# Kernel optimization log

Hardware: AMD Instinct MI355X
Metric: run time of the kernel (lower is better)

Reference implementation:

```python
import jax, jax.numpy as jnp
import numpy as np

D_PAIR = 128
N_HEAD = 4
D_HID = 32
SCALING = 1.0 / np.sqrt(D_HID)


def setup_inputs() -> dict:
    key = jax.random.key(0)
    ks = jax.random.split(key, 12)
    B, L = 1, 256
    s = 0.02
    return {
        "pair": jax.random.normal(ks[0], (B, L, L, D_PAIR), dtype=jnp.float32),
        "gamma": jnp.ones((D_PAIR,), jnp.float32),
        "beta": jnp.zeros((D_PAIR,), jnp.float32),
        "Wq": jax.random.normal(ks[1], (D_PAIR, N_HEAD * D_HID), jnp.float32) * s,
        "Wk": jax.random.normal(ks[2], (D_PAIR, N_HEAD * D_HID), jnp.float32) * s,
        "Wv": jax.random.normal(ks[3], (D_PAIR, N_HEAD * D_HID), jnp.float32) * s,
        "Wb": jax.random.normal(ks[4], (D_PAIR, N_HEAD), jnp.float32) * s,
        "Wg": jax.random.normal(ks[5], (D_PAIR, N_HEAD * D_HID), jnp.float32) * s,
        "bg": jnp.ones((N_HEAD * D_HID,), jnp.float32),
        "Wo": jax.random.normal(ks[6], (N_HEAD * D_HID, D_PAIR), jnp.float32) * s,
        "bo": jnp.zeros((D_PAIR,), jnp.float32),
    }


def _layernorm(x, gamma, beta, eps=1e-5):
    mu = jnp.mean(x, axis=-1, keepdims=True)
    var = jnp.var(x, axis=-1, keepdims=True)
    return (x - mu) * jax.lax.rsqrt(var + eps) * gamma + beta


def reference(pair, gamma, beta, Wq, Wk, Wv, Wb, Wg, bg, Wo, bo):
    B, L = pair.shape[:2]
    x = _layernorm(pair, gamma, beta)                      # (B,L,L,D)
    q = (x @ Wq).reshape(B, L, L, N_HEAD, D_HID) * SCALING  # (B,L,L,h,d)
    k = (x @ Wk).reshape(B, L, L, N_HEAD, D_HID)
    v = (x @ Wv).reshape(B, L, L, N_HEAD, D_HID)
    bias = x @ Wb                                           # (B,L,L,h)
    gate = jax.nn.sigmoid(x @ Wg + bg)                      # (B,L,L,h*d)
    # start_node=True: attend over ending index k of row i
    attn = jnp.einsum('bijhd,bikhd->bijkh', q, k)           # (B,L,L,L,h)
    attn = attn + bias[:, None]                             # bias[b,j,k,h] broadcast over i
    attn = jax.nn.softmax(attn, axis=-2)                    # over k
    out = jnp.einsum('bijkh,bikhd->bijhd', attn, v).reshape(B, L, L, N_HEAD * D_HID)
    out = gate * out
    return out @ Wo + bo
```

## Files before the change

kernel.cpp:

```cpp
#include <hip/hip_runtime.h>
#include <math.h>

#define L 256
#define DP 128
#define NH 4
#define DH 32
#define NROW 65536

typedef unsigned short ushort_t;
typedef __attribute__((ext_vector_type(8))) short short8;
typedef __attribute__((ext_vector_type(4))) float f32x4;
typedef __attribute__((ext_vector_type(4))) unsigned int u32x4;

constexpr float SCALING = 0.17677669529663687f;

static __device__ __forceinline__ unsigned short f2bf(float f) {
    unsigned u = __builtin_bit_cast(unsigned, f);
    u = u + 0x7fffu + ((u >> 16) & 1u);
    return (unsigned short)(u >> 16);
}
static __device__ __forceinline__ float bf2f(unsigned short h) {
    unsigned u = ((unsigned)h) << 16;
    return __builtin_bit_cast(float, u);
}
static __device__ __forceinline__ unsigned packbf(float lo, float hi) {
    return ((unsigned)f2bf(hi) << 16) | (unsigned)f2bf(lo);
}

__global__ __launch_bounds__(256) void prep_kernel(
    const float* __restrict__ Wq, const float* __restrict__ Wk, const float* __restrict__ Wv,
    const float* __restrict__ Wb, const float* __restrict__ Wg, const float* __restrict__ Wo,
    ushort_t* __restrict__ WtAll, ushort_t* __restrict__ WohT, ushort_t* __restrict__ WolT)
{
    int rowi = blockIdx.x * 16 + (threadIdx.x >> 4);
    int d0 = (threadIdx.x & 15) * 8;
    #pragma unroll
    for (int dd = 0; dd < 8; ++dd) {
        int d = d0 + dd;
        if (rowi < 512) {
            int n = rowi & 127;
            float val;
            if (rowi < 128)      val = Wq[d * 128 + n] * SCALING;
            else if (rowi < 256) val = Wk[d * 128 + n];
            else if (rowi < 384) val = Wv[d * 128 + n];
            else                 val = Wg[d * 128 + n];
            WtAll[rowi * 128 + d] = f2bf(val);
        } else if (rowi < 516) {
            WtAll[rowi * 128 + d] = f2bf(Wb[d * 4 + (rowi - 512)]);
        } else if (rowi < 528) {
            WtAll[rowi * 128 + d] = 0;
        } else if (rowi < 656) {
            int n = rowi - 528;
            WohT[n * 128 + d] = f2bf(Wo[d * 128 + n]);
        } else {
            int n = rowi - 656;
            float wv = Wo[d * 128 + n];
            unsigned short hb = f2bf(wv);
            WolT[n * 128 + d] = f2bf(wv - bf2f(hb));
        }
    }
}

__global__ __launch_bounds__(256) void ln_proj_mfma(
    const float* __restrict__ pair, const float* __restrict__ gamma, const float* __restrict__ beta,
    const ushort_t* __restrict__ WtAll, const float* __restrict__ bgv,
    ushort_t* __restrict__ qo, ushort_t* __restrict__ ko, ushort_t* __restrict__ vo,
    ushort_t* __restrict__ gateo, float* __restrict__ biasT)
{
    __shared__ __align__(16) unsigned char xs[32 * 256];

    const int t = threadIdx.x;
    const int w = t >> 6, lane = t & 63;
    const int c = lane & 15, g = lane >> 4;
    const int base = blockIdx.x * 32;

    {
        const float* pr = pair + ((size_t)base + w * 8) * DP;
        float e0[8], e1[8];
        #pragma unroll
        for (int r = 0; r < 8; ++r) {
            e0[r] = pr[r * DP + lane];
            e1[r] = pr[r * DP + 64 + lane];
        }
        const float g0 = gamma[lane], g1 = gamma[lane + 64];
        const float b0 = beta[lane],  b1 = beta[lane + 64];
        #pragma unroll
        for (int r = 0; r < 8; ++r) {
            float s = e0[r] + e1[r], ss = e0[r] * e0[r] + e1[r] * e1[r];
            #pragma unroll
            for (int o = 32; o > 0; o >>= 1) { s += __shfl_xor(s, o); ss += __shfl_xor(ss, o); }
            float mu = s * (1.f / DP);
            float rq = rsqrtf(ss * (1.f / DP) - mu * mu + 1e-5f);
            int rl = w * 8 + r;
            unsigned swz = (unsigned)((rl & 7) << 4);
            *(ushort_t*)(xs + (((unsigned)(rl * 256 + 2 * lane)) ^ swz)) = f2bf((e0[r] - mu) * rq * g0 + b0);
            *(ushort_t*)(xs + (((unsigned)(rl * 256 + 2 * (lane + 64))) ^ swz)) = f2bf((e1[r] - mu) * rq * g1 + b1);
        }
    }
    __syncthreads();

    short8 af[2][4];
    #pragma unroll
    for (int rg = 0; rg < 2; ++rg) {
        const int rl = rg * 16 + c;
        const unsigned swz = (unsigned)((rl & 7) << 4);
        #pragma unroll
        for (int kk = 0; kk < 4; ++kk)
            af[rg][kk] = *(const short8*)(xs + (((unsigned)(rl * 256 + kk * 64 + g * 16)) ^ swz));
    }

    const int mtot = (w == 3) ? 9 : 8;
    for (int m = 0; m < mtot; ++m) {
        const int nt = (m < 8) ? (w + 4 * m) : 32;
        const ushort_t* wbp = WtAll + (size_t)(nt * 16 + c) * 128 + 8 * g;
        short8 bw[4];
        #pragma unroll
        for (int kk = 0; kk < 4; ++kk) bw[kk] = *(const short8*)(wbp + kk * 32);

        const int n = nt * 16 + c;
        #pragma unroll
        for (int rg = 0; rg < 2; ++rg) {
            f32x4 acc = {0.f, 0.f, 0.f, 0.f};
            #pragma unroll
            for (int kk = 0; kk < 4; ++kk)
                acc = __builtin_amdgcn_mfma_f32_16x16x32_bf16(af[rg][kk], bw[kk], acc, 0, 0, 0);

            const int rowb = base + rg * 16 + 4 * g;
            if (nt < 8) {
                #pragma unroll
                for (int e = 0; e < 4; ++e) qo[(size_t)(rowb + e) * 128 + n] = f2bf(acc[e]);
            } else if (nt < 16) {
                #pragma unroll
                for (int e = 0; e < 4; ++e) ko[(size_t)(rowb + e) * 128 + (n - 128)] = f2bf(acc[e]);
            } else if (nt < 24) {
                #pragma unroll
                for (int e = 0; e < 4; ++e) vo[(size_t)(rowb + e) * 128 + (n - 256)] = f2bf(acc[e]);
            } else if (nt < 32) {
                float bgn = bgv[n - 384];
                #pragma unroll
                for (int e = 0; e < 4; ++e)
                    gateo[(size_t)(rowb + e) * 128 + (n - 384)] =
                        f2bf(1.f / (1.f + __expf(-(acc[e] + bgn))));
            } else {
                if (c < 4) {
                    #pragma unroll
                    for (int e = 0; e < 4; ++e)
                        biasT[(size_t)c * NROW + rowb + e] = acc[e];
                }
            }
        }
    }
}

__global__ __launch_bounds__(512) void attn_mfma(
    const ushort_t* __restrict__ qbf, const ushort_t* __restrict__ kbf, const ushort_t* __restrict__ vbf,
    const ushort_t* __restrict__ gbf, const float* __restrict__ biasT,
    ushort_t* __restrict__ xh, ushort_t* __restrict__ xl)
{
    __shared__ __align__(16) unsigned char Kb[256 * 64];
    __shared__ __align__(16) unsigned char Vt[32 * 512];

    const int h = blockIdx.x & 3, i = blockIdx.x >> 2;
    const int t = threadIdx.x, w = t >> 6, lane = t & 63;
    const int c = lane & 15, g = lane >> 4;

    const int j0 = w * 32;
    short8 qf[2];
    {
        const ushort_t* qg = qbf + (size_t)(i * 256 + j0) * 128 + h * 32;
        #pragma unroll
        for (int jt = 0; jt < 2; ++jt)
            qf[jt] = *(const short8*)(qg + (size_t)(jt * 16 + c) * 128 + 8 * g);
    }

    {
        const ushort_t* kg = kbf + (size_t)(i * 256) * 128 + h * 32;
        #pragma unroll
        for (int it = 0; it < 2; ++it) {
            int idx = it * 512 + t;
            int kr = idx >> 2, dp4 = idx & 3;
            *(u32x4*)(Kb + kr * 64 + dp4 * 16) = *(const u32x4*)(kg + (size_t)kr * 128 + dp4 * 8);
        }
    }
    {
        const ushort_t* vg = vbf + (size_t)(i * 256) * 128 + h * 32;
        #pragma unroll
        for (int it = 0; it < 2; ++it) {
            int idx = it * 512 + t;
            int kp = idx >> 3, dp = idx & 7;
            int kt = kp >> 4, cc = kp & 15;
            int a = cc & 3, gg = cc >> 2;
            int k1 = (a < 2) ? (4 * gg + 2 * a) : (12 + 4 * gg + 2 * a);
            int r0 = kt * 32 + k1;
            uint2 va = *(const uint2*)(vg + (size_t)r0 * 128 + dp * 4);
            uint2 vb = *(const uint2*)(vg + (size_t)(r0 + 1) * 128 + dp * 4);
            unsigned av[4] = { va.x & 0xffffu, va.x >> 16, va.y & 0xffffu, va.y >> 16 };
            unsigned bv[4] = { vb.x & 0xffffu, vb.x >> 16, vb.y & 0xffffu, vb.y >> 16 };
            int kcolb = kt * 64 + 4 * cc;
            #pragma unroll
            for (int dd = 0; dd < 4; ++dd) {
                int d = 4 * dp + dd;
                unsigned pk = (bv[dd] << 16) | av[dd];
                *(unsigned*)(Vt + (((unsigned)(d * 512 + kcolb)) ^ ((unsigned)((d & 7) << 4)))) = pk;
            }
        }
    }
    __syncthreads();

    const float* biasH = biasT + (size_t)h * NROW;

    f32x4 O[2][2];
    float rsum[2] = {0.f, 0.f};
    #pragma unroll
    for (int jt = 0; jt < 2; ++jt) {
        O[jt][0] = (f32x4){0.f, 0.f, 0.f, 0.f};
        O[jt][1] = (f32x4){0.f, 0.f, 0.f, 0.f};
    }

    for (int kt = 0; kt < 8; ++kt) {
        short8 kf[2];
        #pragma unroll
        for (int ks = 0; ks < 2; ++ks)
            kf[ks] = *(const short8*)(Kb + (kt * 32 + ks * 16 + c) * 64 + g * 16);
        short8 vb0 = *(const short8*)(Vt + (((unsigned)(c * 512 + kt * 64 + g * 16)) ^ ((unsigned)((c & 7) << 4))));
        short8 vb1 = *(const short8*)(Vt + (((unsigned)((16 + c) * 512 + kt * 64 + g * 16)) ^ ((unsigned)(((16 + c) & 7) << 4))));

        #pragma unroll
        for (int jt = 0; jt < 2; ++jt) {
            f32x4 s0, s1;
            {
                f32x4 z = {0.f, 0.f, 0.f, 0.f};
                s0 = __builtin_amdgcn_mfma_f32_16x16x32_bf16(kf[0], qf[jt], z, 0, 0, 0);
                s1 = __builtin_amdgcn_mfma_f32_16x16x32_bf16(kf[1], qf[jt], z, 0, 0, 0);
            }
            const int jrow = j0 + jt * 16 + c;
            const f32x4 b0 = *(const f32x4*)(biasH + (size_t)jrow * 256 + kt * 32 + 4 * g);
            const f32x4 b1 = *(const f32x4*)(biasH + (size_t)jrow * 256 + kt * 32 + 16 + 4 * g);
            #pragma unroll
            for (int e = 0; e < 4; ++e) {
                s0[e] = __expf(s0[e] + b0[e]);
                s1[e] = __expf(s1[e] + b1[e]);
            }
            rsum[jt] += (s0[0] + s0[1] + s0[2] + s0[3]) + (s1[0] + s1[1] + s1[2] + s1[3]);
            u32x4 pk;
            pk[0] = packbf(s0[0], s0[1]);
            pk[1] = packbf(s0[2], s0[3]);
            pk[2] = packbf(s1[0], s1[1]);
            pk[3] = packbf(s1[2], s1[3]);
            short8 pa = __builtin_bit_cast(short8, pk);
            O[jt][0] = __builtin_amdgcn_mfma_f32_16x16x32_bf16(vb0, pa, O[jt][0], 0, 0, 0);
            O[jt][1] = __builtin_amdgcn_mfma_f32_16x16x32_bf16(vb1, pa, O[jt][1], 0, 0, 0);
        }
    }

    #pragma unroll
    for (int jt = 0; jt < 2; ++jt) {
        float v = rsum[jt];
        v += __shfl_xor(v, 16);
        v += __shfl_xor(v, 32);
        rsum[jt] = 1.f / v;
    }
    const ushort_t* gB = gbf + (size_t)(i * 256 + j0) * 128 + h * 32;
    ushort_t* xhB = xh + (size_t)(i * 256 + j0) * 128 + h * 32;
    ushort_t* xlB = xl + (size_t)(i * 256 + j0) * 128 + h * 32;
    #pragma unroll
    for (int jt = 0; jt < 2; ++jt) {
        const float inv = rsum[jt];
        #pragma unroll
        for (int dt = 0; dt < 2; ++dt) {
            const int off = (jt * 16 + c) * 128 + dt * 16 + 4 * g;
            uint2 gv = *(const uint2*)(gB + off);
            unsigned gs[4] = { gv.x & 0xffffu, gv.x >> 16, gv.y & 0xffffu, gv.y >> 16 };
            float xq[4];
            unsigned short hq[4];
            #pragma unroll
            for (int e = 0; e < 4; ++e) {
                xq[e] = bf2f((unsigned short)gs[e]) * O[jt][dt][e] * inv;
                hq[e] = f2bf(xq[e]);
            }
            uint2 hv, lv;
            hv.x = ((unsigned)hq[1] << 16) | hq[0];
            hv.y = ((unsigned)hq[3] << 16) | hq[2];
            lv.x = packbf(xq[0] - bf2f(hq[0]), xq[1] - bf2f(hq[1]));
            lv.y = packbf(xq[2] - bf2f(hq[2]), xq[3] - bf2f(hq[3]));
            *(uint2*)(xhB + off) = hv;
            *(uint2*)(xlB + off) = lv;
        }
    }
}

__global__ __launch_bounds__(256) void out_proj_mfma(
    const ushort_t* __restrict__ xh, const ushort_t* __restrict__ xl,
    const ushort_t* __restrict__ WohT, const ushort_t* __restrict__ WolT,
    const float* __restrict__ bo, float* __restrict__ out)
{
    const int t = threadIdx.x;
    const int w = t >> 6, lane = t & 63;
    const int c = lane & 15, g = lane >> 4;
    const int base = (blockIdx.x >> 1) * 64;
    const int nh = blockIdx.x & 1;

    const size_t arow = (size_t)(base + w * 16 + c) * 128;
    short8 ah[4], al[4];
    #pragma unroll
    for (int kk = 0; kk < 4; ++kk) {
        ah[kk] = *(const short8*)(xh + arow + kk * 32 + g * 8);
        al[kk] = *(const short8*)(xl + arow + kk * 32 + g * 8);
    }

    const int rowb = base + w * 16 + 4 * g;
    #pragma unroll
    for (int m = 0; m < 4; ++m) {
        const int nt = nh * 4 + m;
        f32x4 acc = {0.f, 0.f, 0.f, 0.f};
        const ushort_t* wh = WohT + (size_t)(nt * 16 + c) * 128 + 8 * g;
        const ushort_t* wl = WolT + (size_t)(nt * 16 + c) * 128 + 8 * g;
        #pragma unroll
        for (int kk = 0; kk < 4; ++kk) {
            short8 bh = *(const short8*)(wh + kk * 32);
            short8 bl = *(const short8*)(wl + kk * 32);
            acc = __builtin_amdgcn_mfma_f32_16x16x32_bf16(ah[kk], bh, acc, 0, 0, 0);
            acc = __builtin_amdgcn_mfma_f32_16x16x32_bf16(ah[kk], bl, acc, 0, 0, 0);
            acc = __builtin_amdgcn_mfma_f32_16x16x32_bf16(al[kk], bh, acc, 0, 0, 0);
        }
        int n = nt * 16 + c;
        float bon = bo[n];
        #pragma unroll
        for (int e = 0; e < 4; ++e)
            out[(size_t)(rowb + e) * 128 + n] = acc[e] + bon;
    }
}

extern "C" void kernel_launch(void* const* d_in, const int* in_sizes, int n_in,
                              void* d_out, int out_size, void* d_ws, size_t ws_size,
                              hipStream_t stream) {
    const float* pair  = (const float*)d_in[0];
    const float* gamma = (const float*)d_in[1];
    const float* beta  = (const float*)d_in[2];
    const float* Wq    = (const float*)d_in[3];
    const float* Wk    = (const float*)d_in[4];
    const float* Wv    = (const float*)d_in[5];
    const float* Wb    = (const float*)d_in[6];
    const float* Wg    = (const float*)d_in[7];
    const float* bg    = (const float*)d_in[8];
    const float* Wo    = (const float*)d_in[9];
    const float* bo    = (const float*)d_in[10];

    unsigned char* ws = (unsigned char*)d_ws;
    size_t off = 0;
    ushort_t* q_bf   = (ushort_t*)(ws + off); off += (size_t)NROW * 128 * 2;
    ushort_t* k_bf   = (ushort_t*)(ws + off); off += (size_t)NROW * 128 * 2;
    ushort_t* v_bf   = (ushort_t*)(ws + off); off += (size_t)NROW * 128 * 2;
    ushort_t* g_bf   = (ushort_t*)(ws + off); off += (size_t)NROW * 128 * 2;
    ushort_t* xh_bf  = (ushort_t*)(ws + off); off += (size_t)NROW * 128 * 2;
    ushort_t* xl_bf  = (ushort_t*)(ws + off); off += (size_t)NROW * 128 * 2;
    float*    biasT  = (float*)(ws + off);    off += (size_t)NH * NROW * 4;
    ushort_t* WtAll  = (ushort_t*)(ws + off); off += 528 * 128 * 2;
    ushort_t* WohT   = (ushort_t*)(ws + off); off += 128 * 128 * 2;
    ushort_t* WolT   = (ushort_t*)(ws + off); off += 128 * 128 * 2;

    prep_kernel<<<49, 256, 0, stream>>>(Wq, Wk, Wv, Wb, Wg, Wo, WtAll, WohT, WolT);
    ln_proj_mfma<<<NROW / 32, 256, 0, stream>>>(pair, gamma, beta, WtAll, bg,
                                                q_bf, k_bf, v_bf, g_bf, biasT);
    attn_mfma<<<L * NH, 512, 0, stream>>>(q_bf, k_bf, v_bf, g_bf, biasT, xh_bf, xl_bf);
    out_proj_mfma<<<NROW / 32, 256, 0, stream>>>(xh_bf, xl_bf, WohT, WolT, bo, (float*)d_out);
}
```

Baseline: 229.5 us.

## Fold log2e into Q and bias, use exp2, seed MFMA with bias, pad K LDS

Folds log2(e) into the Q weight scaling and the stored bias, so the softmax uses the native exp2 instruction instead of __expf. The bias is passed as the MFMA accumulator input, which removes the separate adds. The K shared-memory row stride is padded from 64 to 80 bytes to reduce bank conflicts, and the bf16 conversions now use native __bf16 casts, which may map to hardware packed-convert instructions. The epilogue packing is simplified as well. This trades a little extra LDS for fewer VALU ops in the attention inner loop.

```diff
diff --git a/kernel.cpp b/kernel.cpp
--- a/kernel.cpp
+++ b/kernel.cpp
@@ -11,20 +11,34 @@
 typedef __attribute__((ext_vector_type(8))) short short8;
 typedef __attribute__((ext_vector_type(4))) float f32x4;
 typedef __attribute__((ext_vector_type(4))) unsigned int u32x4;
+typedef __attribute__((ext_vector_type(2))) __bf16 bf16x2;
 
 constexpr float SCALING = 0.17677669529663687f;
+constexpr float LOG2E   = 1.4426950408889634f;
+
+#if __has_builtin(__builtin_amdgcn_exp2f)
+#define EXP2F __builtin_amdgcn_exp2f
+#else
+#define EXP2F exp2f
+#endif
 
 static __device__ __forceinline__ unsigned short f2bf(float f) {
-    unsigned u = __builtin_bit_cast(unsigned, f);
-    u = u + 0x7fffu + ((u >> 16) & 1u);
-    return (unsigned short)(u >> 16);
+    __bf16 h = (__bf16)f;
+    return __builtin_bit_cast(unsigned short, h);
 }
 static __device__ __forceinline__ float bf2f(unsigned short h) {
     unsigned u = ((unsigned)h) << 16;
     return __builtin_bit_cast(float, u);
 }
 static __device__ __forceinline__ unsigned packbf(float lo, float hi) {
-    return ((unsigned)f2bf(hi) << 16) | (unsigned)f2bf(lo);
+    bf16x2 v = {(__bf16)lo, (__bf16)hi};
+    return __builtin_bit_cast(unsigned, v);
+}
+static __device__ __forceinline__ float bf2f_lo(unsigned u) {
+    return __builtin_bit_cast(float, u << 16);
+}
+static __device__ __forceinline__ float bf2f_hi(unsigned u) {
+    return __builtin_bit_cast(float, u & 0xffff0000u);
 }
 
 __global__ __launch_bounds__(256) void prep_kernel(
@@ -40,7 +54,7 @@
         if (rowi < 512) {
             int n = rowi & 127;
             float val;
-            if (rowi < 128)      val = Wq[d * 128 + n] * SCALING;
+            if (rowi < 128)      val = Wq[d * 128 + n] * (SCALING * LOG2E);
             else if (rowi < 256) val = Wk[d * 128 + n];
             else if (rowi < 384) val = Wv[d * 128 + n];
             else                 val = Wg[d * 128 + n];
@@ -145,7 +159,7 @@
                 if (c < 4) {
                     #pragma unroll
                     for (int e = 0; e < 4; ++e)
-                        biasT[(size_t)c * NROW + rowb + e] = acc[e];
+                        biasT[(size_t)c * NROW + rowb + e] = acc[e] * LOG2E;
                 }
             }
         }
@@ -157,7 +171,7 @@
     const ushort_t* __restrict__ gbf, const float* __restrict__ biasT,
     ushort_t* __restrict__ xh, ushort_t* __restrict__ xl)
 {
-    __shared__ __align__(16) unsigned char Kb[256 * 64];
+    __shared__ __align__(16) unsigned char Kb[256 * 80];
     __shared__ __align__(16) unsigned char Vt[32 * 512];
 
     const int h = blockIdx.x & 3, i = blockIdx.x >> 2;
@@ -179,7 +193,7 @@
         for (int it = 0; it < 2; ++it) {
             int idx = it * 512 + t;
             int kr = idx >> 2, dp4 = idx & 3;
-            *(u32x4*)(Kb + kr * 64 + dp4 * 16) = *(const u32x4*)(kg + (size_t)kr * 128 + dp4 * 8);
+            *(u32x4*)(Kb + kr * 80 + dp4 * 16) = *(const u32x4*)(kg + (size_t)kr * 128 + dp4 * 8);
         }
     }
     {
@@ -221,27 +235,23 @@
         short8 kf[2];
         #pragma unroll
         for (int ks = 0; ks < 2; ++ks)
-            kf[ks] = *(const short8*)(Kb + (kt * 32 + ks * 16 + c) * 64 + g * 16);
+            kf[ks] = *(const short8*)(Kb + (kt * 32 + ks * 16 + c) * 80 + g * 16);
         short8 vb0 = *(const short8*)(Vt + (((unsigned)(c * 512 + kt * 64 + g * 16)) ^ ((unsigned)((c & 7) << 4))));
         short8 vb1 = *(const short8*)(Vt + (((unsigned)((16 + c) * 512 + kt * 64 + g * 16)) ^ ((unsigned)(((16 + c) & 7) << 4))));
 
         #pragma unroll
         for (int jt = 0; jt < 2; ++jt) {
-            f32x4 s0, s1;
-            {
-                f32x4 z = {0.f, 0.f, 0.f, 0.f};
-                s0 = __builtin_amdgcn_mfma_f32_16x16x32_bf16(kf[0], qf[jt], z, 0, 0, 0);
-                s1 = __builtin_amdgcn_mfma_f32_16x16x32_bf16(kf[1], qf[jt], z, 0, 0, 0);
-            }
             const int jrow = j0 + jt * 16 + c;
             const f32x4 b0 = *(const f32x4*)(biasH + (size_t)jrow * 256 + kt * 32 + 4 * g);
             const f32x4 b1 = *(const f32x4*)(biasH + (size_t)jrow * 256 + kt * 32 + 16 + 4 * g);
+            f32x4 s0 = __builtin_amdgcn_mfma_f32_16x16x32_bf16(kf[0], qf[jt], b0, 0, 0, 0);
+            f32x4 s1 = __builtin_amdgcn_mfma_f32_16x16x32_bf16(kf[1], qf[jt], b1, 0, 0, 0);
             #pragma unroll
             for (int e = 0; e < 4; ++e) {
-                s0[e] = __expf(s0[e] + b0[e]);
-                s1[e] = __expf(s1[e] + b1[e]);
+                s0[e] = EXP2F(s0[e]);
+                s1[e] = EXP2F(s1[e]);
             }
-            rsum[jt] += (s0[0] + s0[1] + s0[2] + s0[3]) + (s1[0] + s1[1] + s1[2] + s1[3]);
+            rsum[jt] += ((s0[0] + s0[1]) + (s0[2] + s0[3])) + ((s1[0] + s1[1]) + (s1[2] + s1[3]));
             u32x4 pk;
             pk[0] = packbf(s0[0], s0[1]);
             pk[1] = packbf(s0[2], s0[3]);
@@ -270,19 +280,15 @@
         for (int dt = 0; dt < 2; ++dt) {
             const int off = (jt * 16 + c) * 128 + dt * 16 + 4 * g;
             uint2 gv = *(const uint2*)(gB + off);
-            unsigned gs[4] = { gv.x & 0xffffu, gv.x >> 16, gv.y & 0xffffu, gv.y >> 16 };
-            float xq[4];
-            unsigned short hq[4];
-            #pragma unroll
-            for (int e = 0; e < 4; ++e) {
-                xq[e] = bf2f((unsigned short)gs[e]) * O[jt][dt][e] * inv;
-                hq[e] = f2bf(xq[e]);
-            }
-            uint2 hv, lv;
-            hv.x = ((unsigned)hq[1] << 16) | hq[0];
-            hv.y = ((unsigned)hq[3] << 16) | hq[2];
-            lv.x = packbf(xq[0] - bf2f(hq[0]), xq[1] - bf2f(hq[1]));
-            lv.y = packbf(xq[2] - bf2f(hq[2]), xq[3] - bf2f(hq[3]));
+            float x0 = bf2f_lo(gv.x) * O[jt][dt][0] * inv;
+            float x1 = bf2f_hi(gv.x) * O[jt][dt][1] * inv;
+            float x2 = bf2f_lo(gv.y) * O[jt][dt][2] * inv;
+            float x3 = bf2f_hi(gv.y) * O[jt][dt][3] * inv;
+            unsigned h01 = packbf(x0, x1), h23 = packbf(x2, x3);
+            float r0 = x0 - bf2f_lo(h01), r1 = x1 - bf2f_hi(h01);
+            float r2 = x2 - bf2f_lo(h23), r3 = x3 - bf2f_hi(h23);
+            uint2 hv = { h01, h23 };
+            uint2 lv = { packbf(r0, r1), packbf(r2, r3) };
             *(uint2*)(xhB + off) = hv;
             *(uint2*)(xlB + off) = lv;
         }
```

Result: no change. 227.4 us (-0.9%).
